# Optimization experiments

Measured on AMD Instinct MI355X. Metric: run time of the kernel, lower is better.

Reference implementation:

```python
import jax, jax.numpy as jnp
import numpy as np

K = 512
RATE = 0.999

def _l2norm(v):
    # matches torch F.normalize(dim=1): v / max(||v||, 1e-12)
    n = jnp.linalg.norm(v, axis=1, keepdims=True)
    return v / jnp.maximum(n, 1e-12)

def setup_inputs() -> dict:
    key = jax.random.key(0)
    k1, k2 = jax.random.split(key)
    x = jax.random.normal(k1, (16, 256, 64, 64), dtype=jnp.float32)
    m = jax.random.normal(k2, (K, 256), dtype=jnp.float32)
    return {"x": x, "m": m}

def reference(x, m):
    b, c, h, w = x.shape
    xf = x.transpose(0, 2, 3, 1).reshape(-1, c)          # (n, c)
    xn = _l2norm(xf)
    mn = _l2norm(m)
    score = xn @ mn.T                                     # (n, k)
    # EMA codebook update (uses detached x in the original)
    xd = jax.lax.stop_gradient(xf)
    embed_ind = jnp.argmax(score, axis=1)                 # (n,)
    embed_sum = jax.ops.segment_sum(xd, embed_ind, num_segments=K)   # (k, c)
    counts = jax.ops.segment_sum(jnp.ones(xd.shape[0], xd.dtype), embed_ind, num_segments=K)
    embed_mean = embed_sum / (counts[:, None] + 1e-6)
    new_m = m * RATE + embed_mean * (1.0 - RATE)          # (k, c)
    # re-score against updated codebook
    mn2 = _l2norm(new_m)
    score2 = xn @ mn2.T                                   # (n, k)
    soft_label = jax.nn.softmax(score2, axis=1)
    out = soft_label @ new_m                              # (n, c)
    out = out.reshape(b, h, w, c).transpose(0, 3, 1, 2)   # (b, c, h, w)
    return out, score2
```

## Files before the change

### kernel.cpp

```cpp
#include <hip/hip_runtime.h>

#define Bb 16
#define Cc 256
#define HW 4096
#define Nn 65536
#define Kk 512

typedef __attribute__((ext_vector_type(4))) float f32x4;
typedef __attribute__((ext_vector_type(8))) short short8;

__device__ __forceinline__ float bf2f(unsigned int u){
  union { float f; unsigned int i; } v; v.i = u << 16; return v.f;
}
__device__ __forceinline__ unsigned short f2bf(float f){
  unsigned int i = __float_as_uint(f);
  unsigned int r = (i + 0x7fffu + ((i >> 16) & 1u)) >> 16;
  return (unsigned short)r;
}


__global__ __launch_bounds__(64) void k_mnorm(const float* __restrict__ m,
                                              unsigned short* __restrict__ mnf){
  int k = blockIdx.x, l = threadIdx.x;
  float4 v = *reinterpret_cast<const float4*>(m + (size_t)k * Cc + l * 4);
  float ss = v.x*v.x + v.y*v.y + v.z*v.z + v.w*v.w;
  #pragma unroll
  for (int off = 1; off < 64; off <<= 1) ss += __shfl_xor(ss, off, 64);
  float rn = 1.0f / fmaxf(sqrtf(ss), 1e-12f);
  ushort4 o;
  o.x = f2bf(v.x*rn); o.y = f2bf(v.y*rn); o.z = f2bf(v.z*rn); o.w = f2bf(v.w*rn);
  int kw = k >> 6, kt = (k >> 4) & 3, li = k & 15;
  int c0 = l * 4;
  int ks = c0 >> 5, gr = (c0 >> 3) & 3, eo = (l & 1) * 4;
  size_t off8 = ((((size_t)(kw*4 + kt)*8 + ks)*16 + li)*4 + gr)*8 + eo;
  *reinterpret_cast<ushort4*>(mnf + off8) = o;
}

__global__ __launch_bounds__(512, 4) void k_prep_score(const float* __restrict__ x,
                                                       const unsigned short* __restrict__ mnf,
                                                       float* __restrict__ rs,
                                                       unsigned short* __restrict__ xr,
                                                       int* __restrict__ eind){
  __shared__ __align__(16) char ldsB[32768];
  __shared__ float red[8][64];
  __shared__ float smax[8][64];
  __shared__ int   sidx[8][64];
  int t = threadIdx.x, w = t >> 6, l = t & 63, gr = l >> 4, li = l & 15;
  int b = blockIdx.x >> 6;
  int hw0 = (blockIdx.x & 63) << 6;
  const float* src = x + ((size_t)b * Cc + w * 32) * HW + hw0 + l;
  float ss = 0.f;
  unsigned int pk[16];
  #pragma unroll
  for (int j = 0; j < 16; ++j){
    float v0 = src[(size_t)(2*j    ) * HW];
    float v1 = src[(size_t)(2*j + 1) * HW];
    ss += v0 * v0 + v1 * v1;
    pk[j] = (unsigned int)f2bf(v0) | ((unsigned int)f2bf(v1) << 16);
  }
  #pragma unroll
  for (int q = 0; q < 4; ++q){
    int colb = w * 64 + q * 16;
    int4 vv;
    vv.x = (int)pk[q*4+0]; vv.y = (int)pk[q*4+1];
    vv.z = (int)pk[q*4+2]; vv.w = (int)pk[q*4+3];
    *reinterpret_cast<int4*>(ldsB + l * 512 + (colb ^ ((l & 7) << 4))) = vv;
  }
  red[w][l] = ss;
  __syncthreads();
  if (t < 64){
    float s = 0.f;
    #pragma unroll
    for (int ww = 0; ww < 8; ++ww) s += red[ww][t];
    rs[(size_t)b * HW + hw0 + t] = 1.0f / fmaxf(sqrtf(s), 1e-12f);
  }
  f32x4 acc[4][4];
  #pragma unroll
  for (int mt = 0; mt < 4; ++mt)
    #pragma unroll
    for (int nt = 0; nt < 4; ++nt)
      acc[mt][nt] = (f32x4){0.f,0.f,0.f,0.f};
  int loff = li * 32 + gr * 8;
  for (int ks = 0; ks < 8; ++ks){
    short8 af[4];
    #pragma unroll
    for (int mt = 0; mt < 4; ++mt){
      int row = mt * 16 + li;
      af[mt] = *reinterpret_cast<const short8*>(
          ldsB + row * 512 + ((ks * 64 + gr * 16) ^ ((row & 7) << 4)));
    }
    #pragma unroll
    for (int nt = 0; nt < 4; ++nt){
      short8 bv = *reinterpret_cast<const short8*>(
          mnf + ((size_t)(w*4 + nt)*8 + ks)*512 + loff);
      #pragma unroll
      for (int mt = 0; mt < 4; ++mt)
        acc[mt][nt] = __builtin_amdgcn_mfma_f32_16x16x32_bf16(af[mt], bv, acc[mt][nt], 0, 0, 0);
    }
  }
  #pragma unroll
  for (int mt = 0; mt < 4; ++mt){
    #pragma unroll
    for (int r = 0; r < 4; ++r){
      float best = acc[mt][0][r]; int bi = w * 64 + li;
      #pragma unroll
      for (int nt = 1; nt < 4; ++nt){
        float v = acc[mt][nt][r]; int ii = w * 64 + nt * 16 + li;
        if (v > best){ best = v; bi = ii; }
      }
      #pragma unroll
      for (int off = 1; off < 16; off <<= 1){
        float ov = __shfl_xor(best, off, 64);
        int   oi = __shfl_xor(bi,   off, 64);
        if (ov > best || (ov == best && oi < bi)){ best = ov; bi = oi; }
      }
      if (li == 0){ int pr = mt * 16 + gr * 4 + r; smax[w][pr] = best; sidx[w][pr] = bi; }
    }
  }
  __syncthreads();
  if (t < 64){
    float best = smax[0][t]; int bi = sidx[0][t];
    #pragma unroll
    for (int ww = 1; ww < 8; ++ww){
      float v = smax[ww][t]; int ii = sidx[ww][t];
      if (v > best || (v == best && ii < bi)){ best = v; bi = ii; }
    }
    eind[(size_t)b * HW + hw0 + t] = bi;
  }
  char* dst = reinterpret_cast<char*>(xr) + ((size_t)b * HW + hw0) * 512;
  #pragma unroll
  for (int i = 0; i < 4; ++i){
    int px = i * 16 + (t >> 5);
    int colb = (t & 31) * 16;
    int4 rv = *reinterpret_cast<const int4*>(ldsB + px * 512 + (colb ^ ((px & 7) << 4)));
    *reinterpret_cast<int4*>(dst + (size_t)px * 512 + colb) = rv;
  }
}

__global__ __launch_bounds__(256) void k_segsum(const int* __restrict__ eind,
                                                const unsigned short* __restrict__ xr,
                                                float* __restrict__ es4,
                                                float* __restrict__ ec4){
  int kk = blockIdx.x >> 2, qr = blockIdx.x & 3;
  int t = threadIdx.x, w = t >> 6, l = t & 63;
  float a0=0.f,a1=0.f,a2=0.f,a3=0.f;
  int cnt = 0;
  int base = qr * 16384 + w * 4096;
  for (int it = 0; it < 16; ++it){
    int pxb = base + it * 256;
    int4 e = *reinterpret_cast<const int4*>(eind + pxb + l * 4);
    #pragma unroll
    for (int comp = 0; comp < 4; ++comp){
      int ev = comp == 0 ? e.x : comp == 1 ? e.y : comp == 2 ? e.z : e.w;
      unsigned long long mask = __ballot(ev == kk);
      cnt += (int)__popcll(mask);
      while (mask){
        int src = __ffsll((unsigned long long)mask) - 1;
        mask &= mask - 1;
        int px = pxb + src * 4 + comp;
        ushort4 uv = *reinterpret_cast<const ushort4*>(xr + (size_t)px * Cc + l * 4);
        a0 += bf2f(uv.x); a1 += bf2f(uv.y);
        a2 += bf2f(uv.z); a3 += bf2f(uv.w);
      }
    }
  }
  __shared__ float red[4][256];
  __shared__ float rcnt[4];
  red[w][l*4+0]=a0; red[w][l*4+1]=a1; red[w][l*4+2]=a2; red[w][l*4+3]=a3;
  if (l == 0) rcnt[w] = (float)cnt;
  __syncthreads();
  float s = red[0][t] + red[1][t] + red[2][t] + red[3][t];
  es4[(size_t)blockIdx.x * Cc + t] = s;
  if (t == 0) ec4[blockIdx.x] = rcnt[0] + rcnt[1] + rcnt[2] + rcnt[3];
}

__global__ __launch_bounds__(64) void k_update(const float* __restrict__ es4,
                                               const float* __restrict__ ec4,
                                               const float* __restrict__ m,
                                               unsigned short* __restrict__ mn2f,
                                               unsigned short* __restrict__ nmTf){
  int k = blockIdx.x, l = threadIdx.x;
  float sx = 0.f, sy = 0.f, sz = 0.f, sw = 0.f, cs = 0.f;
  #pragma unroll
  for (int q = 0; q < 4; ++q){
    float4 s = *reinterpret_cast<const float4*>(es4 + ((size_t)(4*k+q)) * Cc + l * 4);
    sx += s.x; sy += s.y; sz += s.z; sw += s.w;
    cs += ec4[4*k+q];
  }
  float4 mv = *reinterpret_cast<const float4*>(m + (size_t)k * Cc + l * 4);
  float inv = 1.0f / (cs + 1e-6f);
  float nx = mv.x * 0.999f + sx * inv * 0.001f;
  float ny = mv.y * 0.999f + sy * inv * 0.001f;
  float nz = mv.z * 0.999f + sz * inv * 0.001f;
  float nw = mv.w * 0.999f + sw * inv * 0.001f;
  float ss = nx*nx + ny*ny + nz*nz + nw*nw;
  #pragma unroll
  for (int off = 1; off < 64; off <<= 1) ss += __shfl_xor(ss, off, 64);
  float rn = 1.0f / fmaxf(sqrtf(ss), 1e-12f);
  ushort4 o;
  o.x = f2bf(nx*rn); o.y = f2bf(ny*rn); o.z = f2bf(nz*rn); o.w = f2bf(nw*rn);
  {
    int kw = k >> 6, kt = (k >> 4) & 3, li = k & 15;
    int c0 = l * 4;
    int ks = c0 >> 5, gr = (c0 >> 3) & 3, eo = (l & 1) * 4;
    size_t off8 = ((((size_t)(kw*4 + kt)*8 + ks)*16 + li)*4 + gr)*8 + eo;
    *reinterpret_cast<ushort4*>(mn2f + off8) = o;
  }
  {
    int ksn = k >> 5, grn = (k >> 3) & 3, en = k & 7;
    unsigned short nv[4] = {f2bf(nx), f2bf(ny), f2bf(nz), f2bf(nw)};
    #pragma unroll
    for (int q = 0; q < 4; ++q){
      int c = l * 4 + q;
      int cb = c >> 4, li2 = c & 15;
      size_t off8 = ((((size_t)cb*16 + ksn)*16 + li2)*4 + grn)*8 + en;
      nmTf[off8] = nv[q];
    }
  }
}

__global__ __launch_bounds__(512, 2) void k_out(const unsigned short* __restrict__ xr,
                                                const float* __restrict__ rs,
                                                const unsigned short* __restrict__ mn2f,
                                                const unsigned short* __restrict__ nmTf,
                                                float* __restrict__ out,
                                                float* __restrict__ score2){
  __shared__ __align__(16) char smem[131072];
  __shared__ float wbuf[8 * 128];
  __shared__ float rz[128];
  __shared__ float rsl[128];
  int t = threadIdx.x, w = t >> 6, l = t & 63, gr = l >> 4, li = l & 15;
  int px0 = blockIdx.x * 128;
  const char* gsrc = reinterpret_cast<const char*>(xr + (size_t)px0 * Cc);
  #pragma unroll
  for (int j = 0; j < 8; ++j){
    int chunk = j * 512 + t;
    int rr = chunk >> 5, slot = chunk & 31;
    int4 v = *reinterpret_cast<const int4*>(gsrc + rr * 512 + slot * 16);
    *reinterpret_cast<int4*>(smem + rr * 512 + ((slot * 16) ^ ((rr & 7) << 4))) = v;
  }
  if (t < 128) rsl[t] = rs[px0 + t];
  __syncthreads();
  f32x4 acc[4][8];
  #pragma unroll
  for (int kt = 0; kt < 4; ++kt)
    #pragma unroll
    for (int pt = 0; pt < 8; ++pt)
      acc[kt][pt] = (f32x4){0.f,0.f,0.f,0.f};
  int kw = w * 64;
  int loff = li * 32 + gr * 8;
  for (int ks = 0; ks < 8; ++ks){
    short8 am[4];
    #pragma unroll
    for (int kt = 0; kt < 4; ++kt)
      am[kt] = *reinterpret_cast<const short8*>(
          mn2f + ((size_t)(w*4 + kt)*8 + ks)*512 + loff);
    #pragma unroll
    for (int pt = 0; pt < 8; ++pt){
      int row = pt * 16 + li;
      short8 bx = *reinterpret_cast<const short8*>(
          smem + row * 512 + ((ks * 64 + gr * 16) ^ ((row & 7) << 4)));
      #pragma unroll
      for (int kt = 0; kt < 4; ++kt)
        acc[kt][pt] = __builtin_amdgcn_mfma_f32_16x16x32_bf16(am[kt], bx, acc[kt][pt], 0, 0, 0);
    }
  }
  __syncthreads();
  float s[8] = {0.f,0.f,0.f,0.f,0.f,0.f,0.f,0.f};
  #pragma unroll
  for (int kt = 0; kt < 4; ++kt){
    #pragma unroll
    for (int pt = 0; pt < 8; ++pt){
      int px = pt * 16 + li;
      float rsv = rsl[px];
      f32x4 v = acc[kt][pt];
      v[0] *= rsv; v[1] *= rsv; v[2] *= rsv; v[3] *= rsv;
      acc[kt][pt] = v;
      float p0 = __expf(v[0]), p1 = __expf(v[1]), p2 = __expf(v[2]), p3 = __expf(v[3]);
      s[pt] += (p0 + p1) + (p2 + p3);
      unsigned int lo = (unsigned int)f2bf(p0) | ((unsigned int)f2bf(p1) << 16);
      unsigned int hi = (unsigned int)f2bf(p2) | ((unsigned int)f2bf(p3) << 16);
      int colb = (kw + kt * 16 + gr * 4) * 2;
      uint2 pv; pv.x = lo; pv.y = hi;
      *reinterpret_cast<uint2*>(smem + px * 1024 + (colb ^ ((px & 7) << 4))) = pv;
    }
  }
  #pragma unroll
  for (int pt = 0; pt < 8; ++pt){
    s[pt] += __shfl_xor(s[pt], 16, 64);
    s[pt] += __shfl_xor(s[pt], 32, 64);
  }
  if (gr == 0){
    #pragma unroll
    for (int pt = 0; pt < 8; ++pt) wbuf[w * 128 + pt * 16 + li] = s[pt];
  }
  __syncthreads();
  if (t < 128){
    float sum = 0.f;
    #pragma unroll
    for (int ww = 0; ww < 8; ++ww) sum += wbuf[ww * 128 + t];
    rz[t] = 1.0f / sum;
  }
  float* s2 = score2 + (size_t)px0 * Kk;
  #pragma unroll
  for (int kt = 0; kt < 4; ++kt)
    #pragma unroll
    for (int pt = 0; pt < 8; ++pt){
      int px = pt * 16 + li;
      *reinterpret_cast<f32x4*>(s2 + (size_t)px * Kk + kw + kt * 16 + gr * 4) = acc[kt][pt];
    }
  f32x4 acc2[8][2];
  #pragma unroll
  for (int mt = 0; mt < 8; ++mt)
    #pragma unroll
    for (int nt = 0; nt < 2; ++nt)
      acc2[mt][nt] = (f32x4){0.f,0.f,0.f,0.f};
  for (int ks = 0; ks < 16; ++ks){
    short8 bv[2];
    #pragma unroll
    for (int nt = 0; nt < 2; ++nt)
      bv[nt] = *reinterpret_cast<const short8*>(
          nmTf + ((size_t)(w*2 + nt)*16 + ks)*512 + loff);
    #pragma unroll
    for (int mt = 0; mt < 8; ++mt){
      int row = mt * 16 + li;
      short8 af = *reinterpret_cast<const short8*>(
          smem + row * 1024 + ((ks * 64 + gr * 16) ^ ((row & 7) << 4)));
      #pragma unroll
      for (int nt = 0; nt < 2; ++nt)
        acc2[mt][nt] = __builtin_amdgcn_mfma_f32_16x16x32_bf16(af, bv[nt], acc2[mt][nt], 0, 0, 0);
    }
  }
  __syncthreads();
  int b = px0 >> 12, hw0 = px0 & 4095;
  #pragma unroll
  for (int mt = 0; mt < 8; ++mt){
    int pb = mt * 16 + gr * 4;
    f32x4 rzv = *reinterpret_cast<const f32x4*>(&rz[pb]);
    #pragma unroll
    for (int nt = 0; nt < 2; ++nt){
      int c = w * 32 + nt * 16 + li;
      f32x4 v;
      v[0] = acc2[mt][nt][0] * rzv[0];
      v[1] = acc2[mt][nt][1] * rzv[1];
      v[2] = acc2[mt][nt][2] * rzv[2];
      v[3] = acc2[mt][nt][3] * rzv[3];
      *reinterpret_cast<f32x4*>(out + ((size_t)b * Cc + c) * HW + hw0 + pb) = v;
    }
  }
}

extern "C" void kernel_launch(void* const* d_in, const int* in_sizes, int n_in,
                              void* d_out, int out_size, void* d_ws, size_t ws_size,
                              hipStream_t stream) {
  (void)in_sizes; (void)n_in; (void)out_size; (void)ws_size;
  const float* x = (const float*)d_in[0];
  const float* m = (const float*)d_in[1];
  float* out    = (float*)d_out;
  float* score2 = (float*)d_out + (size_t)Nn * Cc;

  char* ws = (char*)d_ws;
  unsigned short* xr   = (unsigned short*)(ws);
  float*          rsb  = (float*)(ws + 33554432);
  unsigned short* mnf  = (unsigned short*)(ws + 33816576);
  int*            ei   = (int*)(ws + 34078720);
  float*          es4  = (float*)(ws + 34340864);
  float*          ec4  = (float*)(ws + 36438016);
  unsigned short* mn2f = (unsigned short*)(ws + 36446208);
  unsigned short* nmTf = (unsigned short*)(ws + 36708352);

  k_mnorm       <<<512,  64,  0, stream>>>(m, mnf);
  k_prep_score  <<<1024, 512, 0, stream>>>(x, mnf, rsb, xr, ei);
  k_segsum      <<<2048, 256, 0, stream>>>(ei, xr, es4, ec4);
  k_update      <<<512,  64,  0, stream>>>(es4, ec4, m, mn2f, nmTf);
  k_out         <<<512,  512, 0, stream>>>(xr, rsb, mn2f, nmTf, out, score2);
}
```

Before: 158.9 us.

## Split fused score/softmax/output kernel into two kernels via global score2

The single k_out kernel is split into a score kernel that writes score2 and per-pixel softmax reciprocals to global memory, and an output kernel that re-reads score2, recomputes exp, packs bf16 probabilities into LDS and runs the second GEMM. The goal is to shrink LDS in the first kernel, which may raise occupancy, and to simplify each stage's register pressure. The cost is an extra launch and a re-read of the 128 MB score2 tensor plus the repeated exp work.

```diff
diff --git a/kernel.cpp b/kernel.cpp
--- a/kernel.cpp
+++ b/kernel.cpp
@@ -219,15 +219,13 @@
   }
 }
 
-__global__ __launch_bounds__(512, 2) void k_out(const unsigned short* __restrict__ xr,
-                                                const float* __restrict__ rs,
-                                                const unsigned short* __restrict__ mn2f,
-                                                const unsigned short* __restrict__ nmTf,
-                                                float* __restrict__ out,
-                                                float* __restrict__ score2){
-  __shared__ __align__(16) char smem[131072];
+__global__ __launch_bounds__(512, 2) void k5a_score(const unsigned short* __restrict__ xr,
+                                                    const float* __restrict__ rs,
+                                                    const unsigned short* __restrict__ mn2f,
+                                                    float* __restrict__ score2,
+                                                    float* __restrict__ rzg){
+  __shared__ __align__(16) char smem[65536];
   __shared__ float wbuf[8 * 128];
-  __shared__ float rz[128];
   __shared__ float rsl[128];
   int t = threadIdx.x, w = t >> 6, l = t & 63, gr = l >> 4, li = l & 15;
   int px0 = blockIdx.x * 128;
@@ -265,8 +263,8 @@
         acc[kt][pt] = __builtin_amdgcn_mfma_f32_16x16x32_bf16(am[kt], bx, acc[kt][pt], 0, 0, 0);
     }
   }
-  __syncthreads();
   float s[8] = {0.f,0.f,0.f,0.f,0.f,0.f,0.f,0.f};
+  float* s2 = score2 + (size_t)px0 * Kk;
   #pragma unroll
   for (int kt = 0; kt < 4; ++kt){
     #pragma unroll
@@ -275,14 +273,9 @@
       float rsv = rsl[px];
       f32x4 v = acc[kt][pt];
       v[0] *= rsv; v[1] *= rsv; v[2] *= rsv; v[3] *= rsv;
-      acc[kt][pt] = v;
+      *reinterpret_cast<f32x4*>(s2 + (size_t)px * Kk + kw + kt * 16 + gr * 4) = v;
       float p0 = __expf(v[0]), p1 = __expf(v[1]), p2 = __expf(v[2]), p3 = __expf(v[3]);
       s[pt] += (p0 + p1) + (p2 + p3);
-      unsigned int lo = (unsigned int)f2bf(p0) | ((unsigned int)f2bf(p1) << 16);
-      unsigned int hi = (unsigned int)f2bf(p2) | ((unsigned int)f2bf(p3) << 16);
-      int colb = (kw + kt * 16 + gr * 4) * 2;
-      uint2 pv; pv.x = lo; pv.y = hi;
-      *reinterpret_cast<uint2*>(smem + px * 1024 + (colb ^ ((px & 7) << 4))) = pv;
     }
   }
   #pragma unroll
@@ -299,22 +292,41 @@
     float sum = 0.f;
     #pragma unroll
     for (int ww = 0; ww < 8; ++ww) sum += wbuf[ww * 128 + t];
-    rz[t] = 1.0f / sum;
-  }
-  float* s2 = score2 + (size_t)px0 * Kk;
-  #pragma unroll
-  for (int kt = 0; kt < 4; ++kt)
-    #pragma unroll
-    for (int pt = 0; pt < 8; ++pt){
-      int px = pt * 16 + li;
-      *reinterpret_cast<f32x4*>(s2 + (size_t)px * Kk + kw + kt * 16 + gr * 4) = acc[kt][pt];
-    }
+    rzg[px0 + t] = 1.0f / sum;
+  }
+}
+
+__global__ __launch_bounds__(512, 2) void k5b_out(const float* __restrict__ score2,
+                                                  const float* __restrict__ rzg,
+                                                  const unsigned short* __restrict__ nmTf,
+                                                  float* __restrict__ out){
+  __shared__ __align__(16) char ldsP[131072];
+  int t = threadIdx.x, w = t >> 6, l = t & 63, gr = l >> 4, li = l & 15;
+  int px0 = blockIdx.x * 128;
+  const float* s2 = score2 + (size_t)px0 * Kk;
+  #pragma unroll
+  for (int r = 0; r < 16; ++r){
+    int px = w * 16 + r;
+    const float* rowp = s2 + (size_t)px * Kk + l * 8;
+    f32x4 a = reinterpret_cast<const f32x4*>(rowp)[0];
+    f32x4 b2 = reinterpret_cast<const f32x4*>(rowp)[1];
+    float p0 = __expf(a[0]), p1 = __expf(a[1]), p2 = __expf(a[2]), p3 = __expf(a[3]);
+    float p4 = __expf(b2[0]), p5 = __expf(b2[1]), p6 = __expf(b2[2]), p7 = __expf(b2[3]);
+    int4 pv;
+    pv.x = (int)((unsigned int)f2bf(p0) | ((unsigned int)f2bf(p1) << 16));
+    pv.y = (int)((unsigned int)f2bf(p2) | ((unsigned int)f2bf(p3) << 16));
+    pv.z = (int)((unsigned int)f2bf(p4) | ((unsigned int)f2bf(p5) << 16));
+    pv.w = (int)((unsigned int)f2bf(p6) | ((unsigned int)f2bf(p7) << 16));
+    *reinterpret_cast<int4*>(ldsP + px * 1024 + ((l * 16) ^ ((px & 7) << 4))) = pv;
+  }
+  __syncthreads();
   f32x4 acc2[8][2];
   #pragma unroll
   for (int mt = 0; mt < 8; ++mt)
     #pragma unroll
     for (int nt = 0; nt < 2; ++nt)
       acc2[mt][nt] = (f32x4){0.f,0.f,0.f,0.f};
+  int loff = li * 32 + gr * 8;
   for (int ks = 0; ks < 16; ++ks){
     short8 bv[2];
     #pragma unroll
@@ -325,18 +337,17 @@
     for (int mt = 0; mt < 8; ++mt){
       int row = mt * 16 + li;
       short8 af = *reinterpret_cast<const short8*>(
-          smem + row * 1024 + ((ks * 64 + gr * 16) ^ ((row & 7) << 4)));
+          ldsP + row * 1024 + ((ks * 64 + gr * 16) ^ ((row & 7) << 4)));
       #pragma unroll
       for (int nt = 0; nt < 2; ++nt)
         acc2[mt][nt] = __builtin_amdgcn_mfma_f32_16x16x32_bf16(af, bv[nt], acc2[mt][nt], 0, 0, 0);
     }
   }
-  __syncthreads();
   int b = px0 >> 12, hw0 = px0 & 4095;
   #pragma unroll
   for (int mt = 0; mt < 8; ++mt){
     int pb = mt * 16 + gr * 4;
-    f32x4 rzv = *reinterpret_cast<const f32x4*>(&rz[pb]);
+    f32x4 rzv = *reinterpret_cast<const f32x4*>(rzg + px0 + pb);
     #pragma unroll
     for (int nt = 0; nt < 2; ++nt){
       int c = w * 32 + nt * 16 + li;
@@ -368,10 +379,12 @@
   float*          ec4  = (float*)(ws + 36438016);
   unsigned short* mn2f = (unsigned short*)(ws + 36446208);
   unsigned short* nmTf = (unsigned short*)(ws + 36708352);
+  float*          rzg  = (float*)(ws + 36970496);
 
   k_mnorm       <<<512,  64,  0, stream>>>(m, mnf);
   k_prep_score  <<<1024, 512, 0, stream>>>(x, mnf, rsb, xr, ei);
   k_segsum      <<<2048, 256, 0, stream>>>(ei, xr, es4, ec4);
   k_update      <<<512,  64,  0, stream>>>(es4, ec4, m, mn2f, nmTf);
-  k_out         <<<512,  512, 0, stream>>>(xr, rsb, mn2f, nmTf, out, score2);
-}
+  k5a_score     <<<512,  512, 0, stream>>>(xr, rsb, mn2f, score2, rzg);
+  k5b_out       <<<512,  512, 0, stream>>>(score2, rzg, nmTf, out);
+}
```

New measurement: 167.2 us. 1.05x slower.
